# Performance work log

Measured on AMD Instinct MI355X. Metric: run time of the kernel, lower is better.

The kernel has to match this reference:

```python
import jax, jax.numpy as jnp
import numpy as np

N = 100000
E = 3200000
IN_C = 1433
DIM = 32
HEADS = 8
OUT_C = 4
NUM_LAYER = 2
NUM_CLASS = 7
NEG_SLOPE = 0.2


def setup_inputs() -> dict:
    key = jax.random.key(0)
    ks = jax.random.split(key, 12)
    s = 0.05
    return {
        "x": jax.random.normal(ks[0], (N, IN_C), dtype=jnp.float32),
        "edge_index": jax.random.randint(ks[1], (2, E), 0, N, dtype=jnp.int32),
        "w_proj": jax.random.normal(ks[2], (IN_C, DIM), dtype=jnp.float32) * s,
        "b_proj": jnp.zeros((DIM,), dtype=jnp.float32),
        "w_l": jax.random.normal(ks[3], (NUM_LAYER, DIM, HEADS * OUT_C), dtype=jnp.float32) * s,
        "b_l": jnp.zeros((NUM_LAYER, HEADS * OUT_C), dtype=jnp.float32),
        "w_r": jax.random.normal(ks[4], (NUM_LAYER, DIM, HEADS * OUT_C), dtype=jnp.float32) * s,
        "b_r": jnp.zeros((NUM_LAYER, HEADS * OUT_C), dtype=jnp.float32),
        "att": jax.random.normal(ks[5], (NUM_LAYER, HEADS, OUT_C), dtype=jnp.float32) * s,
        "conv_bias": jnp.zeros((NUM_LAYER, HEADS * OUT_C), dtype=jnp.float32),
        "w_pred": jax.random.normal(ks[6], (DIM, NUM_CLASS), dtype=jnp.float32) * s,
        "b_pred": jnp.zeros((NUM_CLASS,), dtype=jnp.float32),
    }


def _gatv2_layer(h, src, dst, wl, bl, wr, br, att, bias):
    # GATv2 (PyG semantics): x_l from source, x_r from target,
    # e = att . leaky_relu(x_l[src] + x_r[dst]); softmax over edges per dst.
    xl = (h @ wl + bl).reshape(N, HEADS, OUT_C)
    xr = (h @ wr + br).reshape(N, HEADS, OUT_C)
    e = jax.nn.leaky_relu(xl[src] + xr[dst], NEG_SLOPE)          # [E, H, C]
    logits = jnp.einsum("ehc,hc->eh", e, att)                    # [E, H]
    m = jax.ops.segment_max(logits, dst, num_segments=N)         # [N, H]
    m = jnp.where(jnp.isfinite(m), m, 0.0)                       # empty segments
    ex = jnp.exp(logits - m[dst])                                # [E, H]
    denom = jax.ops.segment_sum(ex, dst, num_segments=N)         # [N, H]
    alpha = ex / jnp.maximum(denom[dst], 1e-16)                  # [E, H]
    msg = alpha[:, :, None] * xl[src]                            # [E, H, C]
    out = jax.ops.segment_sum(msg, dst, num_segments=N)          # [N, H, C]
    return out.reshape(N, HEADS * OUT_C) + bias


def reference(x, edge_index, w_proj, b_proj, w_l, b_l, w_r, b_r, att, conv_bias, w_pred, b_pred):
    src = edge_index[0]
    dst = edge_index[1]
    h = x @ w_proj + b_proj                                      # [N, DIM]
    for i in range(NUM_LAYER):
        h = h + _gatv2_layer(h, src, dst, w_l[i], b_l[i], w_r[i], b_r[i], att[i], conv_bias[i])
    return h @ w_pred + b_pred                                   # [N, NUM_CLASS]
```

## Files before the change

### kernel.cpp

```cpp
#include <hip/hip_runtime.h>

#define N_NODES 100000
#define N_EDGES 3200000
#define IN_C 1433
#define DIM 32
#define HEADS 8
#define OUT_C 4
#define NUM_CLASS 7

#define KTILES 45
#define N_WAVES 6250
#define PROJ_BLOCKS 1563
#define NB_SCAN 98

typedef __bf16 bf16x8 __attribute__((ext_vector_type(8)));
typedef __bf16 bf16x4 __attribute__((ext_vector_type(4)));
typedef float f32x4 __attribute__((ext_vector_type(4)));

__global__ __launch_bounds__(256) void init_kernel(
    const float* __restrict__ w, bf16x8* __restrict__ wfrag,
    int* __restrict__ cnt) {
  const int g = blockIdx.x * 256 + threadIdx.x;
  if (g < N_NODES) cnt[g] = 0;
  if (blockIdx.x < KTILES * 2 && threadIdx.x < 64) {
    const int kt = blockIdx.x >> 1;
    const int ch = blockIdx.x & 1;
    const int l = threadIdx.x;
    const int col = ch * 16 + (l & 15);
    const int kbase = kt * 32 + (l >> 4) * 8;
    bf16x8 v;
    #pragma unroll
    for (int e = 0; e < 8; ++e) {
      const int k = kbase + e;
      v[e] = (__bf16)((k < IN_C) ? w[(size_t)k * DIM + col] : 0.f);
    }
    wfrag[(size_t)blockIdx.x * 64 + l] = v;
  }
}

__global__ __launch_bounds__(256) void proj_count_kernel(
    const float* __restrict__ x, const bf16x8* __restrict__ wfrag,
    const float* __restrict__ b, float* __restrict__ h,
    const int* __restrict__ dst, int* __restrict__ cnt,
    int* __restrict__ rank) {
  __shared__ float stage[4][16 * 32];
  const int t = threadIdx.x;
  const int lane = t & 63;
  const int wid = t >> 6;
  const int widx = blockIdx.x * 4 + wid;

  if (widx < N_WAVES) {
    const int nodeBase = widx * 16;
    float* slab = stage[wid];

    const int qrow = lane >> 3;
    const int qcol = lane & 7;
    const float* xq = x + (size_t)(nodeBase + qrow) * IN_C + qcol * 4;

    const int frow = lane & 15;
    const int kg = lane >> 4;
    const int sw = frow & 7;
    const int rd0 = frow * 32 + (((2 * kg) ^ sw) << 2);
    const int rd1 = frow * 32 + (((2 * kg + 1) ^ sw) << 2);
    const bf16x8* wp = wfrag + lane;

    f32x4 acc0 = {0.f, 0.f, 0.f, 0.f};
    f32x4 acc1 = {0.f, 0.f, 0.f, 0.f};

    f32x4 cur0 = *(const f32x4*)(xq);
    f32x4 cur1 = *(const f32x4*)(xq + (size_t)8 * IN_C);

    for (int kt = 0; kt < KTILES - 1; ++kt) {
      {
        const int g0 = qcol ^ (qrow & 7);
        *(f32x4*)(slab + qrow * 32 + (g0 << 2)) = cur0;
        const int r1 = qrow + 8;
        const int g1 = qcol ^ (r1 & 7);
        *(f32x4*)(slab + r1 * 32 + (g1 << 2)) = cur1;
      }
      if (kt + 1 < KTILES - 1) {
        const float* xp = xq + (size_t)(kt + 1) * 32;
        cur0 = *(const f32x4*)(xp);
        cur1 = *(const f32x4*)(xp + (size_t)8 * IN_C);
      }
      const f32x4 lo = *(const f32x4*)(slab + rd0);
      const f32x4 hi = *(const f32x4*)(slab + rd1);
      bf16x8 af;
      af[0] = (__bf16)lo[0]; af[1] = (__bf16)lo[1];
      af[2] = (__bf16)lo[2]; af[3] = (__bf16)lo[3];
      af[4] = (__bf16)hi[0]; af[5] = (__bf16)hi[1];
      af[6] = (__bf16)hi[2]; af[7] = (__bf16)hi[3];
      const bf16x8 b0 = wp[(kt * 2 + 0) * 64];
      const bf16x8 b1 = wp[(kt * 2 + 1) * 64];
      acc0 = __builtin_amdgcn_mfma_f32_16x16x32_bf16(af, b0, acc0, 0, 0, 0);
      acc1 = __builtin_amdgcn_mfma_f32_16x16x32_bf16(af, b1, acc1, 0, 0, 0);
    }
    {
      const int srow = lane >> 5;
      const int scol = lane & 31;
      const bool ok = (1408 + scol) < IN_C;
      const float* xt = x + (size_t)(nodeBase + srow) * IN_C + 1408 + scol;
      #pragma unroll
      for (int i = 0; i < 8; ++i) {
        const int row = 2 * i + srow;
        const float v = ok ? xt[(size_t)(2 * i) * IN_C] : 0.f;
        const int p = (scol >> 2) ^ (row & 7);
        slab[row * 32 + (p << 2) + (scol & 3)] = v;
      }
      const f32x4 lo = *(const f32x4*)(slab + rd0);
      const f32x4 hi = *(const f32x4*)(slab + rd1);
      bf16x8 af;
      af[0] = (__bf16)lo[0]; af[1] = (__bf16)lo[1];
      af[2] = (__bf16)lo[2]; af[3] = (__bf16)lo[3];
      af[4] = (__bf16)hi[0]; af[5] = (__bf16)hi[1];
      af[6] = (__bf16)hi[2]; af[7] = (__bf16)hi[3];
      const bf16x8 b0 = wp[((KTILES - 1) * 2 + 0) * 64];
      const bf16x8 b1 = wp[((KTILES - 1) * 2 + 1) * 64];
      acc0 = __builtin_amdgcn_mfma_f32_16x16x32_bf16(af, b0, acc0, 0, 0, 0);
      acc1 = __builtin_amdgcn_mfma_f32_16x16x32_bf16(af, b1, acc1, 0, 0, 0);
    }

    const float bc0 = b[frow];
    const float bc1 = b[frow + 16];
    #pragma unroll
    for (int rg = 0; rg < 4; ++rg) {
      const size_t o = (size_t)(nodeBase + kg * 4 + rg) * DIM + frow;
      h[o] = acc0[rg] + bc0;
      h[o + 16] = acc1[rg] + bc1;
    }
  }

  for (int e = blockIdx.x * 256 + t; e < N_EDGES; e += PROJ_BLOCKS * 256)
    rank[e] = atomicAdd(&cnt[dst[e]], 1);
}

__global__ __launch_bounds__(1024) void scan_local_kernel(
    const int* __restrict__ cnt, int* __restrict__ offs, int* __restrict__ bsum) {
  __shared__ int wsum[16];
  const int t = threadIdx.x;
  const int lane = t & 63;
  const int wid = t >> 6;
  const int idx = blockIdx.x * 1024 + t;
  const int v = (idx < N_NODES) ? cnt[idx] : 0;
  int incl = v;
  #pragma unroll
  for (int off = 1; off < 64; off <<= 1) {
    const int nv = __shfl_up(incl, off, 64);
    if (lane >= off) incl += nv;
  }
  if (lane == 63) wsum[wid] = incl;
  __syncthreads();
  int wpre = 0;
  for (int i = 0; i < wid; ++i) wpre += wsum[i];
  if (idx < N_NODES) offs[idx] = wpre + incl - v;
  if (t == 1023) bsum[blockIdx.x] = wpre + incl;
}

__global__ __launch_bounds__(256) void scan_add_kernel(
    int* __restrict__ offs, const int* __restrict__ bsum) {
  __shared__ int wsum[4];
  const int t = threadIdx.x;
  const int lane = t & 63;
  const int wid = t >> 6;
  const int k = blockIdx.x >> 2;
  int v = (t < k) ? bsum[t] : 0;
  #pragma unroll
  for (int m = 1; m < 64; m <<= 1) v += __shfl_xor(v, m, 64);
  if (lane == 0) wsum[wid] = v;
  __syncthreads();
  const int base = wsum[0] + wsum[1] + wsum[2] + wsum[3];
  const int idx = blockIdx.x * 256 + t;
  if (idx < N_NODES) offs[idx] += base;
  if (idx == 0) offs[N_NODES] = N_EDGES;
}

__global__ __launch_bounds__(256) void scatter_lgemm_kernel(
    const int* __restrict__ src, const int* __restrict__ dst,
    const int* __restrict__ offs, const int* __restrict__ rank,
    int* __restrict__ srcs,
    const float* __restrict__ h,
    const float* __restrict__ wl, const float* __restrict__ bl,
    const float* __restrict__ wr, const float* __restrict__ br,
    __bf16* __restrict__ xlb, float* __restrict__ xr) {
  const int t = threadIdx.x;
  if (blockIdx.x < 12500) {
    const int i = blockIdx.x * 256 + t;
    if (i < N_EDGES) {
      const int d = dst[i];
      srcs[offs[d] + rank[i]] = src[i];
    }
  } else {
    __shared__ float wls[DIM * DIM];
    __shared__ float wrs[DIM * DIM];
    for (int i = t; i < DIM * DIM; i += 256) { wls[i] = wl[i]; wrs[i] = wr[i]; }
    __syncthreads();
    const int node = (blockIdx.x - 12500) * 8 + (t >> 5);
    const int col = t & 31;
    const float* hrow = h + (size_t)node * DIM;
    float al = bl[col], ar = br[col];
    #pragma unroll
    for (int k = 0; k < DIM; ++k) {
      const float hv = hrow[k];
      al += hv * wls[k * DIM + col];
      ar += hv * wrs[k * DIM + col];
    }
    xlb[(size_t)node * DIM + col] = (__bf16)al;
    xr[(size_t)node * DIM + col] = ar;
  }
}

__global__ __launch_bounds__(256) void gat_lgemm_kernel(
    const float* __restrict__ hin, const __bf16* __restrict__ xlb,
    const float* __restrict__ xr, const float* __restrict__ att,
    const float* __restrict__ cbias, const int* __restrict__ offs,
    const int* __restrict__ srcs, float* __restrict__ hout,
    const float* __restrict__ wl1, const float* __restrict__ bl1,
    const float* __restrict__ wr1, const float* __restrict__ br1,
    __bf16* __restrict__ xlbB, float* __restrict__ xrB) {
  __shared__ float wls[DIM * DIM];
  __shared__ float wrs[DIM * DIM];
  const int t = threadIdx.x;
  for (int i = t; i < DIM * DIM; i += 256) { wls[i] = wl1[i]; wrs[i] = wr1[i]; }
  __syncthreads();

  const int lane = t & 63;
  const int node = blockIdx.x * 4 + (t >> 6);
  const int head = lane & 7;
  const int e8 = lane >> 3;
  const float4 a4 = *(const float4*)(att + head * 4);
  const float4 r4 = *(const float4*)(xr + (size_t)node * DIM + head * 4);
  const int beg = offs[node];
  const int end = offs[node + 1];
  float den = 0.f, acc0 = 0.f, acc1 = 0.f, acc2 = 0.f, acc3 = 0.f;
  for (int i = beg + e8; i < end; i += 8) {
    const int s = srcs[i];
    const bf16x4 lb = *(const bf16x4*)(xlb + ((size_t)s << 5) + (head << 2));
    const float l0 = (float)lb[0], l1 = (float)lb[1], l2 = (float)lb[2], l3 = (float)lb[3];
    float e0 = l0 + r4.x; e0 = (e0 > 0.f) ? e0 : 0.2f * e0;
    float e1 = l1 + r4.y; e1 = (e1 > 0.f) ? e1 : 0.2f * e1;
    float e2 = l2 + r4.z; e2 = (e2 > 0.f) ? e2 : 0.2f * e2;
    float e3 = l3 + r4.w; e3 = (e3 > 0.f) ? e3 : 0.2f * e3;
    const float logit = e0 * a4.x + e1 * a4.y + e2 * a4.z + e3 * a4.w;
    const float wgt = __expf(logit);
    den += wgt;
    acc0 += wgt * l0; acc1 += wgt * l1; acc2 += wgt * l2; acc3 += wgt * l3;
  }
  #pragma unroll
  for (int m = 8; m <= 32; m <<= 1) {
    den  += __shfl_xor(den, m, 64);
    acc0 += __shfl_xor(acc0, m, 64);
    acc1 += __shfl_xor(acc1, m, 64);
    acc2 += __shfl_xor(acc2, m, 64);
    acc3 += __shfl_xor(acc3, m, 64);
  }
  const float inv = 1.f / fmaxf(den, 1e-16f);
  const int o = node * DIM + head * 4;
  const float4 hv = *(const float4*)(hin + o);
  const float4 cb = *(const float4*)(cbias + head * 4);
  const float o0 = hv.x + cb.x + acc0 * inv;
  const float o1 = hv.y + cb.y + acc1 * inv;
  const float o2 = hv.z + cb.z + acc2 * inv;
  const float o3 = hv.w + cb.w + acc3 * inv;
  if (lane < 8) {
    float4 outv; outv.x = o0; outv.y = o1; outv.z = o2; outv.w = o3;
    *(float4*)(hout + o) = outv;
  }
  const int col = lane & 31;
  const float* wsel = (lane < 32) ? wls : wrs;
  float a = (lane < 32) ? bl1[col] : br1[col];
  #pragma unroll
  for (int k = 0; k < DIM; ++k) {
    const float src = (k & 3) == 0 ? o0 : (k & 3) == 1 ? o1 : (k & 3) == 2 ? o2 : o3;
    const float hk = __shfl(src, k >> 2, 64);
    a += hk * wsel[k * DIM + col];
  }
  const size_t xo = ((size_t)node << 5) + col;
  if (lane < 32) xlbB[xo] = (__bf16)a;
  else           xrB[xo] = a;
}

__global__ __launch_bounds__(256) void gat_edge_pred_kernel(
    const float* __restrict__ hin, const __bf16* __restrict__ xlb,
    const float* __restrict__ xr, const float* __restrict__ att,
    const float* __restrict__ cbias, const int* __restrict__ offs,
    const int* __restrict__ srcs,
    const float* __restrict__ wp, const float* __restrict__ bp,
    float* __restrict__ out) {
  const int t = threadIdx.x;
  const int lane = t & 63;
  const int node = blockIdx.x * 4 + (t >> 6);
  const int head = lane & 7;
  const int e8 = lane >> 3;
  const float4 a4 = *(const float4*)(att + head * 4);
  const float4 r4 = *(const float4*)(xr + (size_t)node * DIM + head * 4);
  const int beg = offs[node];
  const int end = offs[node + 1];
  float den = 0.f, acc0 = 0.f, acc1 = 0.f, acc2 = 0.f, acc3 = 0.f;
  for (int i = beg + e8; i < end; i += 8) {
    const int s = srcs[i];
    const bf16x4 lb = *(const bf16x4*)(xlb + ((size_t)s << 5) + (head << 2));
    const float l0 = (float)lb[0], l1 = (float)lb[1], l2 = (float)lb[2], l3 = (float)lb[3];
    float e0 = l0 + r4.x; e0 = (e0 > 0.f) ? e0 : 0.2f * e0;
    float e1 = l1 + r4.y; e1 = (e1 > 0.f) ? e1 : 0.2f * e1;
    float e2 = l2 + r4.z; e2 = (e2 > 0.f) ? e2 : 0.2f * e2;
    float e3 = l3 + r4.w; e3 = (e3 > 0.f) ? e3 : 0.2f * e3;
    const float logit = e0 * a4.x + e1 * a4.y + e2 * a4.z + e3 * a4.w;
    const float wgt = __expf(logit);
    den += wgt;
    acc0 += wgt * l0; acc1 += wgt * l1; acc2 += wgt * l2; acc3 += wgt * l3;
  }
  #pragma unroll
  for (int m = 8; m <= 32; m <<= 1) {
    den  += __shfl_xor(den, m, 64);
    acc0 += __shfl_xor(acc0, m, 64);
    acc1 += __shfl_xor(acc1, m, 64);
    acc2 += __shfl_xor(acc2, m, 64);
    acc3 += __shfl_xor(acc3, m, 64);
  }
  const float inv = 1.f / fmaxf(den, 1e-16f);
  const int o = node * DIM + head * 4;
  const float4 hv = *(const float4*)(hin + o);
  const float4 cb = *(const float4*)(cbias + head * 4);
  const float o0 = hv.x + cb.x + acc0 * inv;
  const float o1 = hv.y + cb.y + acc1 * inv;
  const float o2 = hv.z + cb.z + acc2 * inv;
  const float o3 = hv.w + cb.w + acc3 * inv;
  float pj[NUM_CLASS];
  const float* wr0 = wp + (head * 4 + 0) * NUM_CLASS;
  const float* wr1 = wp + (head * 4 + 1) * NUM_CLASS;
  const float* wr2 = wp + (head * 4 + 2) * NUM_CLASS;
  const float* wr3 = wp + (head * 4 + 3) * NUM_CLASS;
  #pragma unroll
  for (int j = 0; j < NUM_CLASS; ++j)
    pj[j] = o0 * wr0[j] + o1 * wr1[j] + o2 * wr2[j] + o3 * wr3[j];
  #pragma unroll
  for (int m = 1; m <= 4; m <<= 1) {
    #pragma unroll
    for (int j = 0; j < NUM_CLASS; ++j) pj[j] += __shfl_xor(pj[j], m, 64);
  }
  if (lane == 0) {
    #pragma unroll
    for (int j = 0; j < NUM_CLASS; ++j)
      out[(size_t)node * NUM_CLASS + j] = pj[j] + bp[j];
  }
}

extern "C" void kernel_launch(void* const* d_in, const int* in_sizes, int n_in,
                              void* d_out, int out_size, void* d_ws, size_t ws_size,
                              hipStream_t stream) {
  const float* x       = (const float*)d_in[0];
  const int*   ei      = (const int*)d_in[1];
  const float* w_proj  = (const float*)d_in[2];
  const float* b_proj  = (const float*)d_in[3];
  const float* w_l     = (const float*)d_in[4];
  const float* b_l     = (const float*)d_in[5];
  const float* w_r     = (const float*)d_in[6];
  const float* b_r     = (const float*)d_in[7];
  const float* att     = (const float*)d_in[8];
  const float* cbias   = (const float*)d_in[9];
  const float* w_pred  = (const float*)d_in[10];
  const float* b_pred  = (const float*)d_in[11];

  const int* e_src = ei;
  const int* e_dst = ei + N_EDGES;

  char* wsp = (char*)d_ws;
  size_t off = 0;
  auto take = [&](size_t bytes) -> void* {
    void* p = wsp + off;
    off += (bytes + 255) & ~(size_t)255;
    return p;
  };
  float*  h0    = (float*)take((size_t)N_NODES * DIM * 4);
  float*  h1    = (float*)take((size_t)N_NODES * DIM * 4);
  __bf16* xlbA  = (__bf16*)take((size_t)N_NODES * DIM * 2);
  float*  xrA   = (float*)take((size_t)N_NODES * DIM * 4);
  __bf16* xlbB  = (__bf16*)take((size_t)N_NODES * DIM * 2);
  float*  xrB   = (float*)take((size_t)N_NODES * DIM * 4);
  int*    offs  = (int*)take((size_t)(N_NODES + 1) * 4);
  int*    cnt   = (int*)take((size_t)N_NODES * 4);
  int*    bsum  = (int*)take((size_t)NB_SCAN * 4);
  int*    srcs  = (int*)take((size_t)N_EDGES * 4);
  int*    rank  = (int*)take((size_t)N_EDGES * 4);
  bf16x8* wfrag = (bf16x8*)take((size_t)KTILES * 2 * 64 * 16);

  init_kernel<<<(N_NODES + 255) / 256, 256, 0, stream>>>(w_proj, wfrag, cnt);
  proj_count_kernel<<<PROJ_BLOCKS, 256, 0, stream>>>(
      x, wfrag, b_proj, h0, e_dst, cnt, rank);
  scan_local_kernel<<<NB_SCAN, 1024, 0, stream>>>(cnt, offs, bsum);
  scan_add_kernel<<<(N_NODES + 255) / 256, 256, 0, stream>>>(offs, bsum);
  scatter_lgemm_kernel<<<25000, 256, 0, stream>>>(
      e_src, e_dst, offs, rank, srcs,
      h0, w_l, b_l, w_r, b_r, xlbA, xrA);
  gat_lgemm_kernel<<<N_NODES / 4, 256, 0, stream>>>(
      h0, xlbA, xrA, att, cbias, offs, srcs, h1,
      w_l + DIM * DIM, b_l + DIM, w_r + DIM * DIM, b_r + DIM, xlbB, xrB);
  gat_edge_pred_kernel<<<N_NODES / 4, 256, 0, stream>>>(
      h1, xlbB, xrB, att + HEADS * OUT_C, cbias + DIM, offs, srcs,
      w_pred, b_pred, (float*)d_out);
}
```

Baseline: 538.6 us.

## Fuse layer-0 left/right linear projections into input projection epilogue via MFMA

The layer-0 x_l/x_r 32x32 GEMMs move out of the scatter kernel and into the epilogue of the input projection kernel. They reuse the just-computed h tile staged in LDS and run as bf16 MFMAs against weight fragments prepared in the init kernel. This removes a re-read of h and a separate block range of scalar FMA work, at the cost of bf16 rounding of h for the layer-0 projection. The edge loops in both GAT kernels also prefetch the next source index one iteration ahead to hide index-load latency.

```diff
diff --git a/kernel.cpp b/kernel.cpp
--- a/kernel.cpp
+++ b/kernel.cpp
@@ -18,7 +18,9 @@
 typedef float f32x4 __attribute__((ext_vector_type(4)));
 
 __global__ __launch_bounds__(256) void init_kernel(
-    const float* __restrict__ w, bf16x8* __restrict__ wfrag,
+    const float* __restrict__ w, const float* __restrict__ wl0,
+    const float* __restrict__ wr0,
+    bf16x8* __restrict__ wfrag, bf16x8* __restrict__ wfrag2,
     int* __restrict__ cnt) {
   const int g = blockIdx.x * 256 + threadIdx.x;
   if (g < N_NODES) cnt[g] = 0;
@@ -35,12 +37,27 @@
       v[e] = (__bf16)((k < IN_C) ? w[(size_t)k * DIM + col] : 0.f);
     }
     wfrag[(size_t)blockIdx.x * 64 + l] = v;
+  } else if (blockIdx.x < KTILES * 2 + 4 && threadIdx.x < 64) {
+    const int bf = blockIdx.x - KTILES * 2;
+    const float* ws = (bf < 2) ? wl0 : wr0;
+    const int ch = bf & 1;
+    const int l = threadIdx.x;
+    const int col = ch * 16 + (l & 15);
+    const int kbase = (l >> 4) * 8;
+    bf16x8 v;
+    #pragma unroll
+    for (int e = 0; e < 8; ++e)
+      v[e] = (__bf16)ws[(size_t)(kbase + e) * DIM + col];
+    wfrag2[(size_t)bf * 64 + l] = v;
   }
 }
 
 __global__ __launch_bounds__(256) void proj_count_kernel(
     const float* __restrict__ x, const bf16x8* __restrict__ wfrag,
-    const float* __restrict__ b, float* __restrict__ h,
+    const bf16x8* __restrict__ wfrag2,
+    const float* __restrict__ b, const float* __restrict__ bl0,
+    const float* __restrict__ br0, float* __restrict__ h,
+    __bf16* __restrict__ xlbA, float* __restrict__ xrA,
     const int* __restrict__ dst, int* __restrict__ cnt,
     int* __restrict__ rank) {
   __shared__ float stage[4][16 * 32];
@@ -124,9 +141,40 @@
     const float bc1 = b[frow + 16];
     #pragma unroll
     for (int rg = 0; rg < 4; ++rg) {
-      const size_t o = (size_t)(nodeBase + kg * 4 + rg) * DIM + frow;
-      h[o] = acc0[rg] + bc0;
-      h[o + 16] = acc1[rg] + bc1;
+      const int nl = kg * 4 + rg;
+      const float o0 = acc0[rg] + bc0;
+      const float o1 = acc1[rg] + bc1;
+      const size_t o = (size_t)(nodeBase + nl) * DIM + frow;
+      h[o] = o0;
+      h[o + 16] = o1;
+      slab[nl * 32 + frow] = o0;
+      slab[nl * 32 + frow + 16] = o1;
+    }
+    {
+      const f32x4 lo = *(const f32x4*)(slab + frow * 32 + kg * 8);
+      const f32x4 hi = *(const f32x4*)(slab + frow * 32 + kg * 8 + 4);
+      bf16x8 af;
+      af[0] = (__bf16)lo[0]; af[1] = (__bf16)lo[1];
+      af[2] = (__bf16)lo[2]; af[3] = (__bf16)lo[3];
+      af[4] = (__bf16)hi[0]; af[5] = (__bf16)hi[1];
+      af[6] = (__bf16)hi[2]; af[7] = (__bf16)hi[3];
+      f32x4 xl0 = {0.f, 0.f, 0.f, 0.f}, xl1 = {0.f, 0.f, 0.f, 0.f};
+      f32x4 xr0 = {0.f, 0.f, 0.f, 0.f}, xr1 = {0.f, 0.f, 0.f, 0.f};
+      xl0 = __builtin_amdgcn_mfma_f32_16x16x32_bf16(af, wfrag2[0 * 64 + lane], xl0, 0, 0, 0);
+      xl1 = __builtin_amdgcn_mfma_f32_16x16x32_bf16(af, wfrag2[1 * 64 + lane], xl1, 0, 0, 0);
+      xr0 = __builtin_amdgcn_mfma_f32_16x16x32_bf16(af, wfrag2[2 * 64 + lane], xr0, 0, 0, 0);
+      xr1 = __builtin_amdgcn_mfma_f32_16x16x32_bf16(af, wfrag2[3 * 64 + lane], xr1, 0, 0, 0);
+      const float bl_0 = bl0[frow], bl_1 = bl0[frow + 16];
+      const float br_0 = br0[frow], br_1 = br0[frow + 16];
+      #pragma unroll
+      for (int rg = 0; rg < 4; ++rg) {
+        const int nl = kg * 4 + rg;
+        const size_t o = ((size_t)(nodeBase + nl) << 5) + frow;
+        xlbA[o] = (__bf16)(xl0[rg] + bl_0);
+        xlbA[o + 16] = (__bf16)(xl1[rg] + bl_1);
+        xrA[o] = xr0[rg] + br_0;
+        xrA[o + 16] = xr1[rg] + br_1;
+      }
     }
   }
 
@@ -174,38 +222,14 @@
   if (idx == 0) offs[N_NODES] = N_EDGES;
 }
 
-__global__ __launch_bounds__(256) void scatter_lgemm_kernel(
+__global__ __launch_bounds__(256) void scatter_kernel(
     const int* __restrict__ src, const int* __restrict__ dst,
     const int* __restrict__ offs, const int* __restrict__ rank,
-    int* __restrict__ srcs,
-    const float* __restrict__ h,
-    const float* __restrict__ wl, const float* __restrict__ bl,
-    const float* __restrict__ wr, const float* __restrict__ br,
-    __bf16* __restrict__ xlb, float* __restrict__ xr) {
-  const int t = threadIdx.x;
-  if (blockIdx.x < 12500) {
-    const int i = blockIdx.x * 256 + t;
-    if (i < N_EDGES) {
-      const int d = dst[i];
-      srcs[offs[d] + rank[i]] = src[i];
-    }
-  } else {
-    __shared__ float wls[DIM * DIM];
-    __shared__ float wrs[DIM * DIM];
-    for (int i = t; i < DIM * DIM; i += 256) { wls[i] = wl[i]; wrs[i] = wr[i]; }
-    __syncthreads();
-    const int node = (blockIdx.x - 12500) * 8 + (t >> 5);
-    const int col = t & 31;
-    const float* hrow = h + (size_t)node * DIM;
-    float al = bl[col], ar = br[col];
-    #pragma unroll
-    for (int k = 0; k < DIM; ++k) {
-      const float hv = hrow[k];
-      al += hv * wls[k * DIM + col];
-      ar += hv * wrs[k * DIM + col];
-    }
-    xlb[(size_t)node * DIM + col] = (__bf16)al;
-    xr[(size_t)node * DIM + col] = ar;
+    int* __restrict__ srcs) {
+  const int i = blockIdx.x * 256 + threadIdx.x;
+  if (i < N_EDGES) {
+    const int d = dst[i];
+    srcs[offs[d] + rank[i]] = src[i];
   }
 }
 
@@ -220,7 +244,7 @@
   __shared__ float wls[DIM * DIM];
   __shared__ float wrs[DIM * DIM];
   const int t = threadIdx.x;
-  for (int i = t; i < DIM * DIM; i += 256) { wls[i] = wl1[i]; wrs[i] = wr1[i]; }
+  for (int i2 = t; i2 < DIM * DIM; i2 += 256) { wls[i2] = wl1[i2]; wrs[i2] = wr1[i2]; }
   __syncthreads();
 
   const int lane = t & 63;
@@ -232,8 +256,11 @@
   const int beg = offs[node];
   const int end = offs[node + 1];
   float den = 0.f, acc0 = 0.f, acc1 = 0.f, acc2 = 0.f, acc3 = 0.f;
-  for (int i = beg + e8; i < end; i += 8) {
-    const int s = srcs[i];
+  int i = beg + e8;
+  int sNext = (i < end) ? srcs[i] : 0;
+  for (; i < end; i += 8) {
+    const int s = sNext;
+    if (i + 8 < end) sNext = srcs[i + 8];
     const bf16x4 lb = *(const bf16x4*)(xlb + ((size_t)s << 5) + (head << 2));
     const float l0 = (float)lb[0], l1 = (float)lb[1], l2 = (float)lb[2], l3 = (float)lb[3];
     float e0 = l0 + r4.x; e0 = (e0 > 0.f) ? e0 : 0.2f * e0;
@@ -296,8 +323,11 @@
   const int beg = offs[node];
   const int end = offs[node + 1];
   float den = 0.f, acc0 = 0.f, acc1 = 0.f, acc2 = 0.f, acc3 = 0.f;
-  for (int i = beg + e8; i < end; i += 8) {
-    const int s = srcs[i];
+  int i = beg + e8;
+  int sNext = (i < end) ? srcs[i] : 0;
+  for (; i < end; i += 8) {
+    const int s = sNext;
+    if (i + 8 < end) sNext = srcs[i + 8];
     const bf16x4 lb = *(const bf16x4*)(xlb + ((size_t)s << 5) + (head << 2));
     const float l0 = (float)lb[0], l1 = (float)lb[1], l2 = (float)lb[2], l3 = (float)lb[3];
     float e0 = l0 + r4.x; e0 = (e0 > 0.f) ? e0 : 0.2f * e0;
@@ -371,27 +401,28 @@
     off += (bytes + 255) & ~(size_t)255;
     return p;
   };
-  float*  h0    = (float*)take((size_t)N_NODES * DIM * 4);
-  float*  h1    = (float*)take((size_t)N_NODES * DIM * 4);
-  __bf16* xlbA  = (__bf16*)take((size_t)N_NODES * DIM * 2);
-  float*  xrA   = (float*)take((size_t)N_NODES * DIM * 4);
-  __bf16* xlbB  = (__bf16*)take((size_t)N_NODES * DIM * 2);
-  float*  xrB   = (float*)take((size_t)N_NODES * DIM * 4);
-  int*    offs  = (int*)take((size_t)(N_NODES + 1) * 4);
-  int*    cnt   = (int*)take((size_t)N_NODES * 4);
-  int*    bsum  = (int*)take((size_t)NB_SCAN * 4);
-  int*    srcs  = (int*)take((size_t)N_EDGES * 4);
-  int*    rank  = (int*)take((size_t)N_EDGES * 4);
-  bf16x8* wfrag = (bf16x8*)take((size_t)KTILES * 2 * 64 * 16);
-
-  init_kernel<<<(N_NODES + 255) / 256, 256, 0, stream>>>(w_proj, wfrag, cnt);
+  float*  h0     = (float*)take((size_t)N_NODES * DIM * 4);
+  float*  h1     = (float*)take((size_t)N_NODES * DIM * 4);
+  __bf16* xlbA   = (__bf16*)take((size_t)N_NODES * DIM * 2);
+  float*  xrA    = (float*)take((size_t)N_NODES * DIM * 4);
+  __bf16* xlbB   = (__bf16*)take((size_t)N_NODES * DIM * 2);
+  float*  xrB    = (float*)take((size_t)N_NODES * DIM * 4);
+  int*    offs   = (int*)take((size_t)(N_NODES + 1) * 4);
+  int*    cnt    = (int*)take((size_t)N_NODES * 4);
+  int*    bsum   = (int*)take((size_t)NB_SCAN * 4);
+  int*    srcs   = (int*)take((size_t)N_EDGES * 4);
+  int*    rank   = (int*)take((size_t)N_EDGES * 4);
+  bf16x8* wfrag  = (bf16x8*)take((size_t)KTILES * 2 * 64 * 16);
+  bf16x8* wfrag2 = (bf16x8*)take((size_t)4 * 64 * 16);
+
+  init_kernel<<<(N_NODES + 255) / 256, 256, 0, stream>>>(
+      w_proj, w_l, w_r, wfrag, wfrag2, cnt);
   proj_count_kernel<<<PROJ_BLOCKS, 256, 0, stream>>>(
-      x, wfrag, b_proj, h0, e_dst, cnt, rank);
+      x, wfrag, wfrag2, b_proj, b_l, b_r, h0, xlbA, xrA, e_dst, cnt, rank);
   scan_local_kernel<<<NB_SCAN, 1024, 0, stream>>>(cnt, offs, bsum);
   scan_add_kernel<<<(N_NODES + 255) / 256, 256, 0, stream>>>(offs, bsum);
-  scatter_lgemm_kernel<<<25000, 256, 0, stream>>>(
-      e_src, e_dst, offs, rank, srcs,
-      h0, w_l, b_l, w_r, b_r, xlbA, xrA);
+  scatter_kernel<<<(N_EDGES + 255) / 256, 256, 0, stream>>>(
+      e_src, e_dst, offs, rank, srcs);
   gat_lgemm_kernel<<<N_NODES / 4, 256, 0, stream>>>(
       h0, xlbA, xrA, att, cbias, offs, srcs, h1,
       w_l + DIM * DIM, b_l + DIM, w_r + DIM * DIM, b_r + DIM, xlbB, xrB);
```

Measured after the change: 505.3 us. 1.07x faster.
